# Kernel tuning notes

Measured on AMD Instinct MI355X. Metric: run time of the kernel, lower is better.

Reference implementation:

```python
import jax, jax.numpy as jnp
import numpy as np

LAMBDA_SOFTMAX = 9.0
EPS = 1e-8


def _l2norm(x, axis):
    # matches torch l2norm: x / (sqrt(sum(x^2)+eps) + eps)
    n = jnp.sqrt(jnp.sum(x * x, axis=axis, keepdims=True) + EPS) + EPS
    return x / n


def setup_inputs() -> dict:
    key = jax.random.key(0)
    k1, k2, k3, k4 = jax.random.split(key, 4)
    n_img, n_cap, n_reg, n_words, d = 128, 128, 36, 48, 1024
    return {
        "img_emb": jax.random.normal(k1, (n_img, n_reg, d), jnp.float32),
        "img_mean": jax.random.normal(k2, (n_img, d), jnp.float32),
        "cap_emb": jax.random.normal(k3, (n_cap, n_words, d), jnp.float32),
        "cap_mean": jax.random.normal(k4, (n_cap, d), jnp.float32),
    }


def reference(img_emb, img_mean, cap_emb, cap_mean):
    # img_emb: [I, R, D]; cap_emb: [C, W, D]
    n_reg = img_emb.shape[1]
    n_words = cap_emb.shape[1]
    # global similarities g[c, i]
    g = cap_mean @ img_mean.T
    # raw dot products S[c, i, r, w] = img_emb[i, r] . cap_emb[c, w]
    S = jnp.einsum('ird,cwd->cirw', img_emb, cap_emb)

    # ---- t2i branch: query=cap (w), context=img (r) ----
    # original attn [i, r, w]: leaky -> l2norm over w -> softmax over r
    a = jax.nn.leaky_relu(S, 0.1)
    a = _l2norm(a, axis=3)
    a = jax.nn.softmax(LAMBDA_SOFTMAX * a, axis=2)
    ra = g[:, :, None, None] * a
    ra = ra / jnp.sum(ra, axis=2, keepdims=True)  # renormalize over source (r)
    # t2i_sim[c, i] = mean_w sum_r ra * S  (since weightedContext.cap = ra contracted with S)
    t2i = jnp.einsum('cirw,cirw->ci', ra, S) / n_words

    # ---- i2t branch: query=img (r), context=cap (w) ----
    # original attn [i, w, r]: leaky -> l2norm over r -> softmax over w
    b = jax.nn.leaky_relu(S, 0.1)
    b = _l2norm(b, axis=2)
    b = jax.nn.softmax(LAMBDA_SOFTMAX * b, axis=3)
    rb = g[:, :, None, None] * b
    rb = rb / jnp.sum(rb, axis=3, keepdims=True)  # renormalize over source (w)
    i2t = jnp.einsum('cirw,cirw->ci', rb, S) / n_reg

    # original returns [n_image, n_caption] (columns appended per caption)
    return (t2i + i2t).T
```

## Files before the change

kernel.cpp:

```cpp
#include <hip/hip_runtime.h>
#include <hip/hip_bf16.h>


#define EPSF 1e-8f
#define LAMF 9.0f

constexpr int IN = 128, CN = 128, RN = 36, WN = 48, DN = 1024;
constexpr size_t NIMG = (size_t)IN * RN * DN;

constexpr int AROWS = 4 * RN;
constexpr int BROWS = 4 * WN;
constexpr int TROWS = AROWS + BROWS;
constexpr int BUFB  = TROWS * 64;

using short8 = __attribute__((ext_vector_type(8))) short;
using f32x4  = __attribute__((ext_vector_type(4))) float;

__device__ __forceinline__ float leaky(float x) { return x > 0.f ? x : 0.1f * x; }

__device__ __forceinline__ unsigned short f2bf(float f) {
    unsigned int b = __float_as_uint(f);
    b += 0x7FFFu + ((b >> 16) & 1u);
    return (unsigned short)(b >> 16);
}

__device__ __forceinline__ void gld_lds16(const unsigned short* g, void* l) {
    __builtin_amdgcn_global_load_lds(
        (const __attribute__((address_space(1))) unsigned int*)g,
        (__attribute__((address_space(3))) unsigned int*)l,
        16, 0, 0);
}

__global__ void cvt_bf16(const float* __restrict__ in, unsigned short* __restrict__ out, int n4) {
    int idx = blockIdx.x * blockDim.x + threadIdx.x;
    if (idx >= n4) return;
    float4 v = ((const float4*)in)[idx];
    ushort4 o;
    o.x = f2bf(v.x); o.y = f2bf(v.y); o.z = f2bf(v.z); o.w = f2bf(v.w);
    ((ushort4*)out)[idx] = o;
}

__global__ __launch_bounds__(256, 3) void scan_mfma(
    const unsigned short* __restrict__ wsb,
    float* __restrict__ out)
{
    __shared__ __align__(16) unsigned char smem[2 * BUFB];
    float (*sS)[RN][WN + 1] = (float (*)[RN][WN + 1])smem;
    float* sncol = (float*)(smem + 28224);
    float* snrow = (float*)(smem + 28992);
    float* scw   = (float*)(smem + 29568);
    float* scr   = (float*)(smem + 30336);

    const int t    = threadIdx.x;
    const int lane = t & 63;
    const int wid  = t >> 6;
    const int lr   = lane & 15;
    const int lg   = lane >> 4;

    const int bi = blockIdx.x;
    const int bc = blockIdx.y;

    unsigned int soff[6];
#pragma unroll
    for (int j = 0; j < 6; ++j) {
        int g = (j < 5) ? (j * 256 + t) : (1280 + t);
        int row = g >> 2, cg = g & 3;
        int sg = cg ^ ((row >> 1) & 3);
        unsigned int off;
        if (row < AROWS)
            off = (unsigned int)((bi * AROWS + row) << 10) + sg * 8;
        else
            off = (unsigned int)NIMG + (unsigned int)((bc * BROWS + (row - AROWS)) << 10) + sg * 8;
        soff[j] = off;
    }

    const int glo = ((lg ^ ((lr >> 1) & 3)) << 4);

    f32x4 acc[9][3];
#pragma unroll
    for (int rt = 0; rt < 9; ++rt)
#pragma unroll
        for (int ct = 0; ct < 3; ++ct) acc[rt][ct] = (f32x4)(0.f);

    auto stage = [&](int bsel, int d0) {
        char* bufp = (char*)smem + bsel * BUFB;
#pragma unroll
        for (int j = 0; j < 5; ++j)
            gld_lds16(wsb + soff[j] + d0, bufp + j * 4096 + wid * 1024);
        if (t < 64)
            gld_lds16(wsb + soff[5] + d0, bufp + 20480);
    };

    stage(0, 0);

    for (int ch = 0; ch < 32; ++ch) {
        __builtin_amdgcn_s_barrier();
        if (ch < 31) {
            stage((ch & 1) ^ 1, (ch + 1) * 32);
            if (wid == 0) asm volatile("s_waitcnt vmcnt(6)" ::: "memory");
            else          asm volatile("s_waitcnt vmcnt(5)" ::: "memory");
        } else {
            asm volatile("s_waitcnt vmcnt(0)" ::: "memory");
        }
        __builtin_amdgcn_s_barrier();
        __builtin_amdgcn_sched_barrier(0);

        const char* bufp = (const char*)smem + (ch & 1) * BUFB;
        const char* ap = bufp + lr * 64 + glo;
        const char* bp = bufp + (AROWS + wid * WN + lr) * 64 + glo;
        short8 b0 = *(const short8*)(bp);
        short8 b1 = *(const short8*)(bp + 1024);
        short8 b2 = *(const short8*)(bp + 2048);

        __builtin_amdgcn_s_setprio(1);
#pragma unroll
        for (int rt = 0; rt < 9; ++rt) {
            short8 a = *(const short8*)(ap + rt * 1024);
            acc[rt][0] = __builtin_amdgcn_mfma_f32_16x16x32_bf16(a, b0, acc[rt][0], 0, 0, 0);
            acc[rt][1] = __builtin_amdgcn_mfma_f32_16x16x32_bf16(a, b1, acc[rt][1], 0, 0, 0);
            acc[rt][2] = __builtin_amdgcn_mfma_f32_16x16x32_bf16(a, b2, acc[rt][2], 0, 0, 0);
        }
        __builtin_amdgcn_s_setprio(0);
    }
    __syncthreads();

#pragma unroll
    for (int r = 0; r < 4; ++r) {
        if (r > 0 && t < 4) {
            float s1 = 0.f, s2 = 0.f;
            for (int w = 0; w < WN; ++w) s1 += scw[t * WN + w];
            for (int rr = 0; rr < RN; ++rr) s2 += scr[t * RN + rr];
            out[(size_t)(bi * 4 + (r - 1)) * CN + (bc * 4 + t)] = s1 / (float)WN + s2 / (float)RN;
        }
#pragma unroll
        for (int rt = 0; rt < 9; ++rt)
#pragma unroll
            for (int reg = 0; reg < 4; ++reg) {
                int lrow = rt * 16 + lg * 4 + reg;
                int ii = lrow / 36;
                if (ii == r) {
                    int rin = lrow - ii * 36;
#pragma unroll
                    for (int ct = 0; ct < 3; ++ct)
                        sS[wid][rin][ct * 16 + lr] = acc[rt][ct][reg];
                }
            }
        __syncthreads();

        if (t < 4 * WN) {
            int tile = t / WN, w = t % WN;
            float ss = 0.f;
            for (int rr = 0; rr < RN; ++rr) { float l = leaky(sS[tile][rr][w]); ss = fmaf(l, l, ss); }
            sncol[t] = LAMF / (sqrtf(ss + EPSF) + EPSF);
        }
        if (t < 4 * RN) {
            int tile = t / RN, rr = t % RN;
            float ss = 0.f;
            for (int w = 0; w < WN; ++w) { float l = leaky(sS[tile][rr][w]); ss = fmaf(l, l, ss); }
            snrow[t] = LAMF / (sqrtf(ss + EPSF) + EPSF);
        }
        __syncthreads();

        if (t < 4 * RN) {
            int tile = t / RN, rr = t % RN;
            const float* Sr = sS[tile][rr];
            const float* ic = sncol + tile * WN;
            float se = 0.f, sw = 0.f;
            for (int w = 0; w < WN; ++w) {
                float s = Sr[w];
                float e = __expf(leaky(s) * ic[w]);
                se += e;
                sw = fmaf(e, s, sw);
            }
            scr[t] = sw / se;
        }
        if (t < 4 * WN) {
            int tile = t / WN, w = t % WN;
            const float* ir = snrow + tile * RN;
            float se = 0.f, sw = 0.f;
            for (int rr = 0; rr < RN; ++rr) {
                float s = sS[tile][rr][w];
                float e = __expf(leaky(s) * ir[rr]);
                se += e;
                sw = fmaf(e, s, sw);
            }
            scw[t] = sw / se;
        }
        __syncthreads();
    }

    if (t < 4) {
        float s1 = 0.f, s2 = 0.f;
        for (int w = 0; w < WN; ++w) s1 += scw[t * WN + w];
        for (int rr = 0; rr < RN; ++rr) s2 += scr[t * RN + rr];
        out[(size_t)(bi * 4 + 3) * CN + (bc * 4 + t)] = s1 / (float)WN + s2 / (float)RN;
    }
}

__global__ __launch_bounds__(256, 4) void scan_fused(
    const float* __restrict__ img_emb, const float* __restrict__ cap_emb,
    float* __restrict__ out)
{
    __shared__ float s_img[48][68];
    __shared__ float s_cap[48][68];
    __shared__ float s_S[RN][WN + 1];
    __shared__ float s_nrow[RN];
    __shared__ float s_ncol[WN];
    __shared__ float s_cw[WN];
    __shared__ float s_cr[RN];

    const int t = threadIdx.x;
    const int c = blockIdx.x & (CN - 1);
    const int i = blockIdx.x >> 7;
    const float* imgB = img_emb + (size_t)i * RN * DN;
    const float* capB = cap_emb + (size_t)c * WN * DN;
    const int ty = t >> 4, tx = t & 15;

    float4 acc[3][3];
#pragma unroll
    for (int a = 0; a < 3; ++a)
#pragma unroll
        for (int b = 0; b < 3; ++b) acc[a][b] = make_float4(0.f, 0.f, 0.f, 0.f);

    for (int d0 = 0; d0 < DN; d0 += 64) {
#pragma unroll
        for (int p = 0; p < 3; ++p) {
            int idx = t + p * 256, row = idx >> 4, col = (idx & 15) << 2;
            float4 v = make_float4(0.f, 0.f, 0.f, 0.f);
            if (row < RN) v = *(const float4*)(imgB + row * DN + d0 + col);
            *(float4*)&s_img[row][col] = v;
        }
#pragma unroll
        for (int p = 0; p < 3; ++p) {
            int idx = t + p * 256, row = idx >> 4, col = (idx & 15) << 2;
            *(float4*)&s_cap[row][col] = *(const float4*)(capB + row * DN + d0 + col);
        }
        __syncthreads();
        for (int d = 0; d < 64; d += 4) {
            float4 a0 = *(float4*)&s_img[ty][d], a1 = *(float4*)&s_img[ty + 16][d], a2 = *(float4*)&s_img[ty + 32][d];
            float4 b0 = *(float4*)&s_cap[tx][d], b1 = *(float4*)&s_cap[tx + 16][d], b2 = *(float4*)&s_cap[tx + 32][d];
#define F4(ac, aa, bb) ac.x=fmaf(aa.x,bb.x,ac.x); ac.y=fmaf(aa.y,bb.y,ac.y); ac.z=fmaf(aa.z,bb.z,ac.z); ac.w=fmaf(aa.w,bb.w,ac.w)
            F4(acc[0][0],a0,b0); F4(acc[0][1],a0,b1); F4(acc[0][2],a0,b2);
            F4(acc[1][0],a1,b0); F4(acc[1][1],a1,b1); F4(acc[1][2],a1,b2);
            F4(acc[2][0],a2,b0); F4(acc[2][1],a2,b1); F4(acc[2][2],a2,b2);
#undef F4
        }
        __syncthreads();
    }
#pragma unroll
    for (int a = 0; a < 3; ++a) {
        int r = ty + 16 * a;
        if (r < RN)
#pragma unroll
            for (int b = 0; b < 3; ++b) {
                float4 v = acc[a][b];
                s_S[r][tx + 16 * b] = (v.x + v.y) + (v.z + v.w);
            }
    }
    __syncthreads();
    if (t < RN) {
        float ss = 0.f;
        for (int w = 0; w < WN; ++w) { float l = leaky(s_S[t][w]); ss = fmaf(l, l, ss); }
        s_nrow[t] = sqrtf(ss + EPSF) + EPSF;
    } else if (t >= 64 && t < 64 + WN) {
        int w = t - 64; float ss = 0.f;
        for (int r = 0; r < RN; ++r) { float l = leaky(s_S[r][w]); ss = fmaf(l, l, ss); }
        s_ncol[w] = sqrtf(ss + EPSF) + EPSF;
    }
    __syncthreads();
    if (t < RN) {
        float se = 0.f, sw = 0.f;
        for (int w = 0; w < WN; ++w) {
            float e = __expf(LAMF * leaky(s_S[t][w]) / s_ncol[w]);
            se += e; sw = fmaf(e, s_S[t][w], sw);
        }
        s_cr[t] = sw / se;
    } else if (t >= 64 && t < 64 + WN) {
        int w = t - 64;
        float se = 0.f, sw = 0.f;
        for (int r = 0; r < RN; ++r) {
            float e = __expf(LAMF * leaky(s_S[r][w]) / s_nrow[r]);
            se += e; sw = fmaf(e, s_S[r][w], sw);
        }
        s_cw[w] = sw / se;
    }
    __syncthreads();
    if (t == 0) {
        float t2i = 0.f, i2t = 0.f;
        for (int w = 0; w < WN; ++w) t2i += s_cw[w];
        for (int r = 0; r < RN; ++r) i2t += s_cr[r];
        out[(size_t)i * CN + c] = t2i / (float)WN + i2t / (float)RN;
    }
}

extern "C" void kernel_launch(void* const* d_in, const int* in_sizes, int n_in,
                              void* d_out, int out_size, void* d_ws, size_t ws_size,
                              hipStream_t stream) {
    const float* img = (const float*)d_in[0];
    const float* cap = (const float*)d_in[2];
    float* out = (float*)d_out;

    const size_t n_img = NIMG;
    const size_t n_cap = (size_t)CN * WN * DN;
    const size_t need  = (n_img + n_cap) * 2;

    if (ws_size >= need) {
        unsigned short* imgh = (unsigned short*)d_ws;
        unsigned short* caph = imgh + n_img;
        int n4i = (int)(n_img / 4), n4c = (int)(n_cap / 4);
        hipLaunchKernelGGL(cvt_bf16, dim3((n4i + 255) / 256), dim3(256), 0, stream, img, imgh, n4i);
        hipLaunchKernelGGL(cvt_bf16, dim3((n4c + 255) / 256), dim3(256), 0, stream, cap, caph, n4c);
        hipLaunchKernelGGL(scan_mfma, dim3(IN / 4, CN / 4), dim3(256), 0, stream, imgh, out);
    } else {
        hipLaunchKernelGGL(scan_fused, dim3(IN * CN), dim3(256), 0, stream, img, cap, out);
    }
}
```

Before: 103.6 us.

## Split MFMA tile across 12 waves and process eight pair tiles per epilogue pass

The block grows from 4 to 12 waves. Each wave now computes a 3x3 grid of 16x16 MFMA tiles (48 rows by 48 columns) instead of 9x3, which cuts accumulator registers per wave and raises waves per CU. Staging loads are spread over more threads. The epilogue handles 8 image-caption pair tiles per pass in two passes instead of four passes of 4, so more of the threads do softmax work. In exchange, the kernel uses more LDS per block and adds barrier cost across more waves.

```diff
diff --git a/kernel.cpp b/kernel.cpp
--- a/kernel.cpp
+++ b/kernel.cpp
@@ -40,30 +40,32 @@
     ((ushort4*)out)[idx] = o;
 }
 
-__global__ __launch_bounds__(256, 3) void scan_mfma(
+__global__ __launch_bounds__(768, 6) void scan_mfma(
     const unsigned short* __restrict__ wsb,
     float* __restrict__ out)
 {
-    __shared__ __align__(16) unsigned char smem[2 * BUFB];
+    __shared__ __align__(16) unsigned char smem[61824];
     float (*sS)[RN][WN + 1] = (float (*)[RN][WN + 1])smem;
-    float* sncol = (float*)(smem + 28224);
-    float* snrow = (float*)(smem + 28992);
-    float* scw   = (float*)(smem + 29568);
-    float* scr   = (float*)(smem + 30336);
+    float* sncol = (float*)(smem + 56448);
+    float* snrow = (float*)(smem + 57984);
+    float* scw   = (float*)(smem + 59136);
+    float* scr   = (float*)(smem + 60672);
 
     const int t    = threadIdx.x;
     const int lane = t & 63;
     const int wid  = t >> 6;
     const int lr   = lane & 15;
     const int lg   = lane >> 4;
+    const int wrt  = wid % 3;
+    const int wct  = wid / 3;
 
     const int bi = blockIdx.x;
     const int bc = blockIdx.y;
 
-    unsigned int soff[6];
-#pragma unroll
-    for (int j = 0; j < 6; ++j) {
-        int g = (j < 5) ? (j * 256 + t) : (1280 + t);
+    unsigned int soff[2];
+#pragma unroll
+    for (int j = 0; j < 2; ++j) {
+        int g = j * 768 + t;
         int row = g >> 2, cg = g & 3;
         int sg = cg ^ ((row >> 1) & 3);
         unsigned int off;
@@ -75,20 +77,20 @@
     }
 
     const int glo = ((lg ^ ((lr >> 1) & 3)) << 4);
-
-    f32x4 acc[9][3];
-#pragma unroll
-    for (int rt = 0; rt < 9; ++rt)
+    const int aoff = (wrt * 48 + lr) * 64 + glo;
+    const int boff = (AROWS + wct * 48 + lr) * 64 + glo;
+
+    f32x4 acc[3][3];
+#pragma unroll
+    for (int rt = 0; rt < 3; ++rt)
 #pragma unroll
         for (int ct = 0; ct < 3; ++ct) acc[rt][ct] = (f32x4)(0.f);
 
     auto stage = [&](int bsel, int d0) {
         char* bufp = (char*)smem + bsel * BUFB;
-#pragma unroll
-        for (int j = 0; j < 5; ++j)
-            gld_lds16(wsb + soff[j] + d0, bufp + j * 4096 + wid * 1024);
-        if (t < 64)
-            gld_lds16(wsb + soff[5] + d0, bufp + 20480);
+        gld_lds16(wsb + soff[0] + d0, bufp + wid * 1024);
+        if (t < 576)
+            gld_lds16(wsb + soff[1] + d0, bufp + 12288 + wid * 1024);
     };
 
     stage(0, 0);
@@ -97,8 +99,8 @@
         __builtin_amdgcn_s_barrier();
         if (ch < 31) {
             stage((ch & 1) ^ 1, (ch + 1) * 32);
-            if (wid == 0) asm volatile("s_waitcnt vmcnt(6)" ::: "memory");
-            else          asm volatile("s_waitcnt vmcnt(5)" ::: "memory");
+            if (wid < 9) asm volatile("s_waitcnt vmcnt(2)" ::: "memory");
+            else         asm volatile("s_waitcnt vmcnt(1)" ::: "memory");
         } else {
             asm volatile("s_waitcnt vmcnt(0)" ::: "memory");
         }
@@ -106,54 +108,61 @@
         __builtin_amdgcn_sched_barrier(0);
 
         const char* bufp = (const char*)smem + (ch & 1) * BUFB;
-        const char* ap = bufp + lr * 64 + glo;
-        const char* bp = bufp + (AROWS + wid * WN + lr) * 64 + glo;
+        const char* ap = bufp + aoff;
+        const char* bp = bufp + boff;
+        short8 a0 = *(const short8*)(ap);
+        short8 a1 = *(const short8*)(ap + 1024);
+        short8 a2 = *(const short8*)(ap + 2048);
         short8 b0 = *(const short8*)(bp);
         short8 b1 = *(const short8*)(bp + 1024);
         short8 b2 = *(const short8*)(bp + 2048);
 
         __builtin_amdgcn_s_setprio(1);
-#pragma unroll
-        for (int rt = 0; rt < 9; ++rt) {
-            short8 a = *(const short8*)(ap + rt * 1024);
-            acc[rt][0] = __builtin_amdgcn_mfma_f32_16x16x32_bf16(a, b0, acc[rt][0], 0, 0, 0);
-            acc[rt][1] = __builtin_amdgcn_mfma_f32_16x16x32_bf16(a, b1, acc[rt][1], 0, 0, 0);
-            acc[rt][2] = __builtin_amdgcn_mfma_f32_16x16x32_bf16(a, b2, acc[rt][2], 0, 0, 0);
-        }
+        acc[0][0] = __builtin_amdgcn_mfma_f32_16x16x32_bf16(a0, b0, acc[0][0], 0, 0, 0);
+        acc[0][1] = __builtin_amdgcn_mfma_f32_16x16x32_bf16(a0, b1, acc[0][1], 0, 0, 0);
+        acc[0][2] = __builtin_amdgcn_mfma_f32_16x16x32_bf16(a0, b2, acc[0][2], 0, 0, 0);
+        acc[1][0] = __builtin_amdgcn_mfma_f32_16x16x32_bf16(a1, b0, acc[1][0], 0, 0, 0);
+        acc[1][1] = __builtin_amdgcn_mfma_f32_16x16x32_bf16(a1, b1, acc[1][1], 0, 0, 0);
+        acc[1][2] = __builtin_amdgcn_mfma_f32_16x16x32_bf16(a1, b2, acc[1][2], 0, 0, 0);
+        acc[2][0] = __builtin_amdgcn_mfma_f32_16x16x32_bf16(a2, b0, acc[2][0], 0, 0, 0);
+        acc[2][1] = __builtin_amdgcn_mfma_f32_16x16x32_bf16(a2, b1, acc[2][1], 0, 0, 0);
+        acc[2][2] = __builtin_amdgcn_mfma_f32_16x16x32_bf16(a2, b2, acc[2][2], 0, 0, 0);
         __builtin_amdgcn_s_setprio(0);
     }
     __syncthreads();
 
 #pragma unroll
-    for (int r = 0; r < 4; ++r) {
-        if (r > 0 && t < 4) {
+    for (int r = 0; r < 2; ++r) {
+        if (r == 1 && t < 8) {
             float s1 = 0.f, s2 = 0.f;
             for (int w = 0; w < WN; ++w) s1 += scw[t * WN + w];
             for (int rr = 0; rr < RN; ++rr) s2 += scr[t * RN + rr];
-            out[(size_t)(bi * 4 + (r - 1)) * CN + (bc * 4 + t)] = s1 / (float)WN + s2 / (float)RN;
-        }
-#pragma unroll
-        for (int rt = 0; rt < 9; ++rt)
+            out[(size_t)(bi * 4 + (t >> 2)) * CN + (bc * 4 + (t & 3))] =
+                s1 / (float)WN + s2 / (float)RN;
+        }
+#pragma unroll
+        for (int rt = 0; rt < 3; ++rt)
 #pragma unroll
             for (int reg = 0; reg < 4; ++reg) {
-                int lrow = rt * 16 + lg * 4 + reg;
+                int lrow = wrt * 48 + rt * 16 + lg * 4 + reg;
                 int ii = lrow / 36;
-                if (ii == r) {
+                if ((ii >> 1) == r) {
+                    int tile = (ii & 1) * 4 + wct;
                     int rin = lrow - ii * 36;
 #pragma unroll
                     for (int ct = 0; ct < 3; ++ct)
-                        sS[wid][rin][ct * 16 + lr] = acc[rt][ct][reg];
+                        sS[tile][rin][ct * 16 + lr] = acc[rt][ct][reg];
                 }
             }
         __syncthreads();
 
-        if (t < 4 * WN) {
+        if (t < 8 * WN) {
             int tile = t / WN, w = t % WN;
             float ss = 0.f;
             for (int rr = 0; rr < RN; ++rr) { float l = leaky(sS[tile][rr][w]); ss = fmaf(l, l, ss); }
             sncol[t] = LAMF / (sqrtf(ss + EPSF) + EPSF);
         }
-        if (t < 4 * RN) {
+        if (t < 8 * RN) {
             int tile = t / RN, rr = t % RN;
             float ss = 0.f;
             for (int w = 0; w < WN; ++w) { float l = leaky(sS[tile][rr][w]); ss = fmaf(l, l, ss); }
@@ -161,7 +170,7 @@
         }
         __syncthreads();
 
-        if (t < 4 * RN) {
+        if (t < 8 * RN) {
             int tile = t / RN, rr = t % RN;
             const float* Sr = sS[tile][rr];
             const float* ic = sncol + tile * WN;
@@ -174,7 +183,7 @@
             }
             scr[t] = sw / se;
         }
-        if (t < 4 * WN) {
+        if (t < 8 * WN) {
             int tile = t / WN, w = t % WN;
             const float* ir = snrow + tile * RN;
             float se = 0.f, sw = 0.f;
@@ -189,11 +198,12 @@
         __syncthreads();
     }
 
-    if (t < 4) {
+    if (t < 8) {
         float s1 = 0.f, s2 = 0.f;
         for (int w = 0; w < WN; ++w) s1 += scw[t * WN + w];
         for (int rr = 0; rr < RN; ++rr) s2 += scr[t * RN + rr];
-        out[(size_t)(bi * 4 + 3) * CN + (bc * 4 + t)] = s1 / (float)WN + s2 / (float)RN;
+        out[(size_t)(bi * 4 + 2 + (t >> 2)) * CN + (bc * 4 + (t & 3))] =
+            s1 / (float)WN + s2 / (float)RN;
     }
 }
 
@@ -310,7 +320,7 @@
         int n4i = (int)(n_img / 4), n4c = (int)(n_cap / 4);
         hipLaunchKernelGGL(cvt_bf16, dim3((n4i + 255) / 256), dim3(256), 0, stream, img, imgh, n4i);
         hipLaunchKernelGGL(cvt_bf16, dim3((n4c + 255) / 256), dim3(256), 0, stream, cap, caph, n4c);
-        hipLaunchKernelGGL(scan_mfma, dim3(IN / 4, CN / 4), dim3(256), 0, stream, imgh, out);
+        hipLaunchKernelGGL(scan_mfma, dim3(IN / 4, CN / 4), dim3(768), 0, stream, imgh, out);
     } else {
         hipLaunchKernelGGL(scan_fused, dim3(IN * CN), dim3(256), 0, stream, img, cap, out);
     }
```

After: 97.27 us (median of 2 runs). 6.2% less time.
